# Kernel optimization log

Measured on AMD Instinct MI355X. Metric: run time of the kernel, lower is better.

Reference implementation:

```python
import jax, jax.numpy as jnp
from jax import lax
import numpy as np

# Config mirroring init_kwargs
B, N, PD = 4, 16384, 3
PROJ = 64                 # projection_channel
M1, K1, C1 = 2048, 32, 128  # level-1 SA: fps points, neighbors, out channel
M2, K2, C2 = 512, 32, 256   # level-2 SA
DH, DO = 512, 256           # dense hidden / out (dense_channels)


def fps(pts, M):
    """Farthest point sampling. pts: [N,3] -> indices [M] (starts at point 0)."""
    n = pts.shape[0]
    def step(carry, _):
        dmin, last = carry
        d = jnp.sum((pts - pts[last]) ** 2, axis=-1)   # dist to newest center
        dmin = jnp.minimum(dmin, d)
        nxt = jnp.argmax(dmin).astype(jnp.int32)
        return (dmin, nxt), last
    init = (jnp.full((n,), 1e10, pts.dtype), jnp.int32(0))
    _, idxs = lax.scan(step, init, None, length=M)
    return idxs


def sa_level(pts, feats, M, K, Wa, ba, Wb, bb):
    """PointNet++ set abstraction: FPS + kNN (xyz space) + grouped MLP + max."""
    idx = jax.vmap(lambda p: fps(p, M))(pts)                       # [B,M]
    centers = jnp.take_along_axis(pts, idx[:, :, None], axis=1)    # [B,M,3]
    d = jnp.sum((centers[:, :, None, :] - pts[:, None, :, :]) ** 2, -1)  # [B,M,N]
    _, nidx = lax.top_k(-d, K)                                      # [B,M,K]
    gather = jax.vmap(lambda a, i: a[i])
    rel = gather(pts, nidx) - centers[:, :, None, :]                # [B,M,K,3]
    nf = gather(feats, nidx)                                        # [B,M,K,C]
    g = jnp.concatenate([rel, nf], axis=-1)                         # use_xyz=True
    h = jax.nn.relu(g @ Wa + ba)
    h = jax.nn.relu(h @ Wb + bb)
    return centers, jnp.max(h, axis=2)                              # [B,M,Cout]


def setup_inputs() -> dict:
    key = jax.random.key(0)
    ks = jax.random.split(key, 12)
    w = lambda k, shape, s: jax.random.normal(k, shape, jnp.float32) * s
    z = lambda c: jnp.zeros((c,), jnp.float32)
    return {
        "xyz": jax.random.normal(ks[0], (B, N, PD), jnp.float32),
        "Wp": w(ks[1], (PD, PROJ), 0.3), "bp": z(PROJ),
        "W1a": w(ks[2], (PROJ + 3, C1), 0.1), "b1a": z(C1),
        "W1b": w(ks[3], (C1, C1), 0.08), "b1b": z(C1),
        "W2a": w(ks[4], (C1 + 3, C2), 0.08), "b2a": z(C2),
        "W2b": w(ks[5], (C2, C2), 0.06), "b2b": z(C2),
        "Wd1": w(ks[6], (2 * C2, DH), 0.05), "bd1": z(DH),
        "Wd2": w(ks[7], (DH, DO), 0.05), "bd2": z(DO),
    }


def reference(xyz, Wp, bp, W1a, b1a, W1b, b1b, W2a, b2a, W2b, b2b,
              Wd1, bd1, Wd2, bd2):
    feats = xyz @ Wp + bp            # point_proj: [B,N,PROJ]
    pts = xyz[..., :3]
    pts, feats = sa_level(pts, feats, M1, K1, W1a, b1a, W1b, b1b)
    pts, feats = sa_level(pts, feats, M2, K2, W2a, b2a, W2b, b2b)
    # global max + avg pool (adaptive_max/avg_pool1d to 1), concat -> [B,2*C2]
    g = jnp.concatenate([jnp.max(feats, axis=1), jnp.mean(feats, axis=1)], -1)
    h = jax.nn.relu(g @ Wd1 + bd1)   # DenseBlock w/ activation
    return h @ Wd2 + bd2             # last block: no activation (last_activation=False)
```

## Files before the change

### kernel.cpp

```cpp
#include <hip/hip_runtime.h>

#define B_    4
#define N1_   16384
#define M1_   2048
#define M2_   512
#define KNN_  32
#define PROJ_ 64
#define C1_   128
#define C2_   256
#define PROJ_BLKS_ ((B_ * N1_ * PROJ_) / 512)
#define KNN_BLKS_  ((M1_ / 64) * (B_ * 64))

__device__ __forceinline__ float sqdist_exact(float px, float py, float pz,
                                              float cx, float cy, float cz) {
    float dx = __fsub_rn(px, cx);
    float dy = __fsub_rn(py, cy);
    float dz = __fsub_rn(pz, cz);
    return __fadd_rn(__fadd_rn(__fmul_rn(dx, dx), __fmul_rn(dy, dy)), __fmul_rn(dz, dz));
}

__device__ __forceinline__ float aload(const float* p) {
    return __uint_as_float(__hip_atomic_load((const unsigned*)p,
                           __ATOMIC_RELAXED, __HIP_MEMORY_SCOPE_AGENT));
}
__device__ __forceinline__ unsigned auload(const unsigned* p) {
    return __hip_atomic_load(p, __ATOMIC_RELAXED, __HIP_MEMORY_SCOPE_AGENT);
}

#define F_PROG1(f,b) ((f) + (b) * 16)
#define F_PROG2(f,b) ((f) + 64 + (b) * 16)
#define F_M2DONE(f,b) ((f) + 128 + (b) * 16)

__global__ void __launch_bounds__(1024)
sortx_kernel(const float* __restrict__ xyz, float* __restrict__ sx,
             float* __restrict__ sy, float* __restrict__ sz,
             float* __restrict__ sp) {
    const int b = blockIdx.x, t = threadIdx.x;
    const int lane = t & 63, w = t >> 6;
    const float* P = xyz + (size_t)b * N1_ * 3;
    __shared__ int hist[1024];
    __shared__ int wsum[16];
    hist[t] = 0;
    __syncthreads();
    for (int j = t; j < N1_; j += 1024) {
        unsigned kb = __float_as_uint(P[j * 3]);
        kb ^= (kb >> 31) ? 0xFFFFFFFFu : 0x80000000u;
        atomicAdd(&hist[kb >> 22], 1);
    }
    __syncthreads();
    int v = hist[t];
    int cum = v;
    for (int off = 1; off < 64; off <<= 1) {
        int o = __shfl_up(cum, off);
        if (lane >= off) cum += o;
    }
    if (lane == 63) wsum[w] = cum;
    __syncthreads();
    int wpre = 0;
    for (int i = 0; i < w; ++i) wpre += wsum[i];
    const int excl = cum - v + wpre;
    __syncthreads();
    hist[t] = excl;
    __syncthreads();
    for (int j = t; j < N1_; j += 1024) {
        float x = P[j * 3], y = P[j * 3 + 1], z = P[j * 3 + 2];
        unsigned kb = __float_as_uint(x);
        kb ^= (kb >> 31) ? 0xFFFFFFFFu : 0x80000000u;
        int pos = atomicAdd(&hist[kb >> 22], 1);
        size_t o = (size_t)b * N1_ + pos;
        sx[o] = x; sy[o] = y; sz[o] = z;
        float* pr = sp + ((size_t)b * N1_ + pos) * 3;
        pr[0] = x; pr[1] = y; pr[2] = z;
    }
}

typedef float v2f __attribute__((ext_vector_type(2)));

template<int CTRL, int RM>
__device__ __forceinline__ unsigned long long dpp_umax64(unsigned long long pk) {
    unsigned lo = (unsigned)__builtin_amdgcn_update_dpp(
        0, (int)(unsigned)pk, CTRL, RM, 0xf, true);
    unsigned hi = (unsigned)__builtin_amdgcn_update_dpp(
        0, (int)(unsigned)(pk >> 32), CTRL, RM, 0xf, true);
    unsigned long long o = ((unsigned long long)hi << 32) | (unsigned long long)lo;
    return (o > pk) ? o : pk;
}

__device__ __forceinline__ unsigned long long wave_max_key(unsigned long long pk) {
    pk = dpp_umax64<0x111, 0xf>(pk);
    pk = dpp_umax64<0x112, 0xf>(pk);
    pk = dpp_umax64<0x114, 0xf>(pk);
    pk = dpp_umax64<0x118, 0xf>(pk);
    pk = dpp_umax64<0x142, 0xa>(pk);
    pk = dpp_umax64<0x143, 0xc>(pk);
    return pk;
}

__device__ __forceinline__ unsigned reduce8_widx(const unsigned long long* wk,
                                                 int lane) {
    unsigned long long k8 = wk[lane & 7];
    k8 = dpp_umax64<0x111, 0xf>(k8);
    k8 = dpp_umax64<0x112, 0xf>(k8);
    k8 = dpp_umax64<0x114, 0xf>(k8);
    unsigned lo = (unsigned)__builtin_amdgcn_readlane((int)(unsigned)k8, 7);
    return ~lo;
}

__device__ __forceinline__ unsigned reduce2_widx(const unsigned long long* wk,
                                                 int lane) {
    unsigned long long k2 = wk[lane & 1];
    k2 = dpp_umax64<0x111, 0xf>(k2);
    unsigned lo = (unsigned)__builtin_amdgcn_readlane((int)(unsigned)k2, 1);
    return ~lo;
}

template<int N, int NT>
__device__ void knn_bodyT(const float* __restrict__ P,
                          float cx, float cy, float cz,
                          int* __restrict__ out, char* arena) {
    constexpr int K = KNN_;
    constexpr int CAP = 224;
    const int t = threadIdx.x;
    const int lane = t & 63;
    const int w = t >> 6;

    int*      hist = (int*)arena;
    unsigned* eqk  = (unsigned*)(arena + 8192);
    int*      eqi  = (int*)(arena + 8192 + 896);
    int*      wsum = (int*)(arena + 8192 + 1792);
    int*      ctrl = (int*)(arena + 8192 + 1824);

    unsigned prefix = 0; int pbits = 0;
    unsigned Tlo = 0; unsigned long long Thi = 0x100000000ull;
    int L = 0, target = K, Cbin = N;

    for (int round = 0; round < 3; ++round) {
        const int bits  = (round < 2) ? 11 : 10;
        const int nbins = 1 << bits;
        const int shift = 32 - pbits - bits;
        for (int i = t; i < nbins; i += NT) hist[i] = 0;
        __syncthreads();
        for (int j = t; j < N; j += NT) {
            float d = sqdist_exact(P[j * 3], P[j * 3 + 1], P[j * 3 + 2], cx, cy, cz);
            unsigned key = __float_as_uint(d);
            if (key >= Tlo && (unsigned long long)key < Thi)
                atomicAdd(&hist[(key >> shift) & (nbins - 1)], 1);
        }
        __syncthreads();
        const int per = nbins / NT;
        int s = 0;
        for (int i = 0; i < per; ++i) s += hist[t * per + i];
        int cum = s;
        for (int off = 1; off < 64; off <<= 1) {
            int o = __shfl_up(cum, off);
            if (lane >= off) cum += o;
        }
        if (lane == 63) wsum[w] = cum;
        __syncthreads();
        int wpre = 0;
        for (int i = 0; i < w; ++i) wpre += wsum[i];
        cum += wpre;
        const int cumex = cum - s;
        if ((cumex < target) && (cum >= target)) {
            int acc = cumex;
            for (int i = 0; i < per; ++i) {
                int h = hist[t * per + i];
                if (acc + h >= target) { ctrl[2] = t * per + i; ctrl[3] = acc; ctrl[4] = h; break; }
                acc += h;
            }
        }
        __syncthreads();
        const int binsel = ctrl[2];
        const int Ladd   = ctrl[3];
        const int bincnt = ctrl[4];
        L += Ladd;
        target -= Ladd;
        prefix = (prefix << bits) | (unsigned)binsel;
        pbits += bits;
        Tlo = prefix << (32 - pbits);
        Thi = ((unsigned long long)prefix + 1ull) << (32 - pbits);
        Cbin = bincnt;
        __syncthreads();
        if (Cbin <= CAP) break;
    }

    if (t == 0) { ctrl[0] = 0; ctrl[1] = 0; }
    __syncthreads();

    if (Cbin <= CAP) {
        for (int j = t; j < N; j += NT) {
            float d = sqdist_exact(P[j * 3], P[j * 3 + 1], P[j * 3 + 2], cx, cy, cz);
            unsigned key = __float_as_uint(d);
            if (key < Tlo) {
                int p = atomicAdd(&ctrl[0], 1);
                out[p] = j;
            } else if ((unsigned long long)key < Thi) {
                int p = atomicAdd(&ctrl[1], 1);
                eqk[p] = key; eqi[p] = j;
            }
        }
        __syncthreads();
        const int E = ctrl[1];
        for (int e = t; e < E; e += NT) {
            unsigned ke = eqk[e]; int ie = eqi[e];
            int rank = 0;
            for (int f = 0; f < E; ++f) {
                unsigned kf = eqk[f]; int jf = eqi[f];
                rank += (kf < ke || (kf == ke && jf < ie)) ? 1 : 0;
            }
            if (rank < target) out[L + rank] = ie;
        }
    } else {
        if (t < 64) {
            int cnt = 0;
            for (int jb = 0; jb < N; jb += 64) {
                int j = jb + lane;
                float d = sqdist_exact(P[j * 3], P[j * 3 + 1], P[j * 3 + 2], cx, cy, cz);
                unsigned key = __float_as_uint(d);
                if (key < Tlo) {
                    int p = atomicAdd(&ctrl[0], 1);
                    out[p] = j;
                }
                bool eq = (key == Tlo);
                unsigned long long mb = __ballot(eq);
                int below = __popcll(mb & ((1ull << lane) - 1ull));
                if (eq && (cnt + below) < target) out[L + cnt + below] = j;
                cnt += (int)__popcll(mb);
            }
        }
    }
}

__global__ __attribute__((amdgpu_flat_work_group_size(512, 512)))
__attribute__((amdgpu_waves_per_eu(2, 2)))
void mega1_kernel(const float* __restrict__ xyz,
                  const float* __restrict__ sx, const float* __restrict__ sy,
                  const float* __restrict__ sz, const float* __restrict__ sp,
                  const float* __restrict__ Wp, const float* __restrict__ bp,
                  float* __restrict__ feats0, float* __restrict__ centers1,
                  int* __restrict__ nidx1, unsigned* __restrict__ prog) {
#pragma clang fp contract(off)
    __shared__ alignas(16) char arena[24832];
    asm volatile("" ::: "v255");
    const int bid = blockIdx.x;
    const int t = threadIdx.x;

    if (bid >= B_ + PROJ_BLKS_) {
        const int k = bid - (B_ + PROJ_BLKS_);
        const int c = k >> 8;
        const int b = (k >> 6) & 3;
        const int m = c * 64 + (k & 63);
        if (t == 0) {
            while (auload(F_PROG1(prog, b)) <= (unsigned)c)
                __builtin_amdgcn_s_sleep(16);
        }
        __syncthreads();
        const float* cw = centers1 + ((size_t)b * M1_ + m) * 3;
        float cx = aload(cw + 0), cy = aload(cw + 1), cz = aload(cw + 2);
        knn_bodyT<N1_, 512>(xyz + (size_t)b * N1_ * 3, cx, cy, cz,
                            nidx1 + ((size_t)b * M1_ + m) * KNN_, arena);
        return;
    }
    if (bid >= B_) {
        int tid = (bid - B_) * 512 + t;
        int cc = tid & (PROJ_ - 1);
        int pn = tid >> 6;
        const float* p = xyz + (size_t)pn * 3;
        float acc = p[0] * Wp[0 * PROJ_ + cc];
        acc = __fmaf_rn(p[1], Wp[1 * PROJ_ + cc], acc);
        acc = __fmaf_rn(p[2], Wp[2 * PROJ_ + cc], acc);
        feats0[tid] = acc + bp[cc];
        return;
    }
    constexpr int NT = 512;
    constexpr int NW = NT / 64;
    constexpr int PPT = N1_ / NT;
    const int b = bid;
    const int w = t >> 6;
    const int lane = t & 63;
    const float* P  = xyz + (size_t)b * N1_ * 3;
    const float* SX = sx + (size_t)b * N1_;
    const float* SY = sy + (size_t)b * N1_;
    const float* SZ = sz + (size_t)b * N1_;
    const float* SP = sp + (size_t)b * N1_ * 3;
    float* C1 = centers1 + (size_t)b * M1_ * 3;
    const int base = t * PPT;
    const unsigned nbase = ~(unsigned)base;

    unsigned long long (*wkey)[NW] = (unsigned long long(*)[NW])arena;
    float* cb1 = (float*)(arena + 128);

    float px[PPT], py[PPT], pz[PPT], dmin[PPT];
#pragma unroll
    for (int k = 0; k < PPT; ++k) {
        px[k] = SX[base + k];
        py[k] = SY[base + k];
        pz[k] = SZ[base + k];
        dmin[k] = 1e10f;
    }
#pragma unroll
    for (int k = 0; k < PPT; ++k)
        asm volatile("" : "+v"(px[k]), "+v"(py[k]), "+v"(pz[k]), "+v"(dmin[k]));

    float xlo = px[0], xhi = px[0];
#pragma unroll
    for (int k = 1; k < PPT; ++k) {
        xlo = fminf(xlo, px[k]);
        xhi = fmaxf(xhi, px[k]);
    }
    for (int off = 1; off < 64; off <<= 1) {
        xlo = fminf(xlo, __shfl_xor(xlo, off));
        xhi = fmaxf(xhi, __shfl_xor(xhi, off));
    }

    unsigned long long mykey = ((unsigned long long)__float_as_uint(1e10f) << 32);
    float cx = P[0], cy = P[1], cz = P[2];

    for (int m = 0; m < M1_; ++m) {
        if (t == 0) {
            cb1[m * 3 + 0] = cx; cb1[m * 3 + 1] = cy; cb1[m * 3 + 2] = cz;
        }
        if ((m & 63) == 63) {
            __syncthreads();
            const int c = m >> 6;
            if (t < 48)
                ((float4*)C1)[c * 48 + t] = ((const float4*)cb1)[c * 48 + t];
            __syncthreads();
            if (t == 0)
                __hip_atomic_store(F_PROG1(prog, b), (unsigned)(c + 1),
                                   __ATOMIC_RELEASE, __HIP_MEMORY_SCOPE_AGENT);
        }
        if (m == M1_ - 1) break;
        const int par = m & 1;
        const float UBval = __uint_as_float((unsigned)(mykey >> 32));
        const float dxs = fmaxf(fmaxf(xlo - cx, cx - xhi), 0.0f);
        if (!(0.999f * (dxs * dxs) >= UBval)) {
            unsigned long long pk = 0;
#pragma unroll
            for (int k = 0; k < PPT; ++k) {
                float d  = sqdist_exact(px[k], py[k], pz[k], cx, cy, cz);
                float nd = fminf(dmin[k], d);
                dmin[k] = nd;
                unsigned long long kk =
                    ((unsigned long long)__float_as_uint(nd) << 32) |
                    (unsigned)(nbase - (unsigned)k);
                pk = (kk > pk) ? kk : pk;
            }
            pk = wave_max_key(pk);
            unsigned klo = (unsigned)__builtin_amdgcn_readlane((int)(unsigned)pk, 63);
            unsigned khi = (unsigned)__builtin_amdgcn_readlane((int)(unsigned)(pk >> 32), 63);
            mykey = ((unsigned long long)khi << 32) | klo;
        }
        if (lane == 63) wkey[par][w] = mykey;
        __syncthreads();
        const unsigned widx = reduce8_widx(wkey[par], lane);
        const float* cp = SP + (size_t)widx * 3;
        cx = cp[0]; cy = cp[1]; cz = cp[2];
    }
}

__device__ __forceinline__ void fps2_body(const float* __restrict__ centers1,
                                          float* __restrict__ centers2,
                                          unsigned* __restrict__ prog,
                                          char* arena) {
#pragma clang fp contract(off)
    constexpr int NT = 128;
    constexpr int NW = 2;
    constexpr int NP = (M1_ / NT) / 2;
    const int b = blockIdx.x;
    const int t = threadIdx.x;
    const int w = t >> 6;
    const int lane = t & 63;
    const float* P = centers1 + (size_t)b * M1_ * 3;
    float* C = centers2 + (size_t)b * M2_ * 3;

    unsigned long long (*wkey)[NW] = (unsigned long long(*)[NW])arena;
    float* cb2 = (float*)(arena + 64);

    v2f px2[NP], py2[NP], pz2[NP];
    float dmin[2 * NP];
#pragma unroll
    for (int p = 0; p < NP; ++p) {
        const int j0 = (2 * p) * NT + t;
        const int j1 = j0 + NT;
        px2[p] = (v2f){P[j0 * 3 + 0], P[j1 * 3 + 0]};
        py2[p] = (v2f){P[j0 * 3 + 1], P[j1 * 3 + 1]};
        pz2[p] = (v2f){P[j0 * 3 + 2], P[j1 * 3 + 2]};
        dmin[2 * p] = 1e10f; dmin[2 * p + 1] = 1e10f;
    }
#pragma unroll
    for (int p = 0; p < NP; ++p)
        asm volatile("" : "+v"(px2[p]), "+v"(py2[p]), "+v"(pz2[p]));

    float cx = P[0], cy = P[1], cz = P[2];

    for (int m = 0; m < M2_; ++m) {
        if (t == 0) {
            cb2[m * 3 + 0] = cx; cb2[m * 3 + 1] = cy; cb2[m * 3 + 2] = cz;
        }
        if ((m & 63) == 63) {
            __syncthreads();
            const int c = m >> 6;
            if (t < 48)
                ((float4*)C)[c * 48 + t] = ((const float4*)cb2)[c * 48 + t];
            __syncthreads();
            if (t == 0)
                __hip_atomic_store(F_PROG2(prog, b), (unsigned)(c + 1),
                                   __ATOMIC_RELEASE, __HIP_MEMORY_SCOPE_AGENT);
        }
        if (m == M2_ - 1) break;
        const int par = m & 1;
        const v2f c2x = {cx, cx}, c2y = {cy, cy}, c2z = {cz, cz};
        float bv = -1.0f; int bk = 0;
#pragma unroll
        for (int p = 0; p < NP; ++p) {
            v2f dx = px2[p] - c2x;
            v2f dy = py2[p] - c2y;
            v2f dz = pz2[p] - c2z;
            v2f d2 = (dx * dx + dy * dy) + dz * dz;
            float nd0 = fminf(dmin[2 * p],     d2.x);
            float nd1 = fminf(dmin[2 * p + 1], d2.y);
            dmin[2 * p]     = nd0;
            dmin[2 * p + 1] = nd1;
            bool g0 = nd0 > bv; bv = g0 ? nd0 : bv; bk = g0 ? 2 * p     : bk;
            bool g1 = nd1 > bv; bv = g1 ? nd1 : bv; bk = g1 ? 2 * p + 1 : bk;
        }
        unsigned gi = (unsigned)(bk * NT + t);
        unsigned long long pk =
            ((unsigned long long)__float_as_uint(bv) << 32) | (unsigned)(~gi);
        pk = wave_max_key(pk);
        if (lane == 63) wkey[par][w] = pk;
        __syncthreads();
        const unsigned widx = reduce2_widx(wkey[par], lane);
        const float* cp = P + (size_t)widx * 3;
        cx = cp[0]; cy = cp[1]; cz = cp[2];
    }
}

template<int NPTS, int FD, int CO, int M>
__device__ __forceinline__ void mlp_body(int bm, char* arena,
                 const float* __restrict__ pts, const float* __restrict__ feats,
                 const float* __restrict__ centers, const int* __restrict__ nidx,
                 const float* __restrict__ Wa, const float* __restrict__ ba,
                 const float* __restrict__ Wb, const float* __restrict__ bb,
                 float* __restrict__ outf) {
    constexpr int KN = KNN_;
    constexpr int GS = FD + 4;
    const int b = bm / M;
    const int t = threadIdx.x;
    float (*g)[GS]  = (float(*)[GS])arena;
    float (*h1)[CO] = (float(*)[CO])(arena + sizeof(float) * KN * GS);
    const int* nb = nidx + (size_t)bm * KN;
    const float* cen = centers + (size_t)bm * 3;
    const float cx = cen[0], cy = cen[1], cz = cen[2];
    {
        constexpr int PARTS = CO / KN;
        constexpr int CHUNK = FD / PARTS;
        const int kk = t / PARTS;
        const int q  = t % PARTS;
        const int j  = nb[kk];
        const float* f = feats + ((size_t)b * NPTS + j) * FD + q * CHUNK;
        float* gr = &g[kk][q * CHUNK];
#pragma unroll
        for (int u = 0; u < CHUNK / 4; ++u)
            *(float4*)(gr + 4 * u) = *(const float4*)(f + 4 * u);
        if (q == 0) {
            const float* p = pts + ((size_t)b * NPTS + j) * 3;
            g[kk][FD + 0] = __fsub_rn(p[0], cx);
            g[kk][FD + 1] = __fsub_rn(p[1], cy);
            g[kk][FD + 2] = __fsub_rn(p[2], cz);
            g[kk][FD + 3] = 0.f;
        }
    }
    __syncthreads();
    const int o = t;
    float acc[KN];
#pragma unroll
    for (int k = 0; k < KN; ++k) acc[k] = ba[o];
    for (int s4 = 0; s4 < FD / 4; ++s4) {
        const float w0 = Wa[(4 * s4 + 3) * CO + o];
        const float w1 = Wa[(4 * s4 + 4) * CO + o];
        const float w2 = Wa[(4 * s4 + 5) * CO + o];
        const float w3 = Wa[(4 * s4 + 6) * CO + o];
#pragma unroll
        for (int k = 0; k < KN; ++k) {
            float4 gv = *(const float4*)&g[k][4 * s4];
            acc[k] = __fmaf_rn(gv.x, w0, acc[k]);
            acc[k] = __fmaf_rn(gv.y, w1, acc[k]);
            acc[k] = __fmaf_rn(gv.z, w2, acc[k]);
            acc[k] = __fmaf_rn(gv.w, w3, acc[k]);
        }
    }
    {
        const float w0 = Wa[0 * CO + o];
        const float w1 = Wa[1 * CO + o];
        const float w2 = Wa[2 * CO + o];
#pragma unroll
        for (int k = 0; k < KN; ++k) {
            float4 gv = *(const float4*)&g[k][FD];
            acc[k] = __fmaf_rn(gv.x, w0, acc[k]);
            acc[k] = __fmaf_rn(gv.y, w1, acc[k]);
            acc[k] = __fmaf_rn(gv.z, w2, acc[k]);
        }
    }
#pragma unroll
    for (int k = 0; k < KN; ++k) h1[k][o] = fmaxf(acc[k], 0.f);
    __syncthreads();
#pragma unroll
    for (int k = 0; k < KN; ++k) acc[k] = bb[o];
    for (int s4 = 0; s4 < CO / 4; ++s4) {
        const float w0 = Wb[(4 * s4 + 0) * CO + o];
        const float w1 = Wb[(4 * s4 + 1) * CO + o];
        const float w2 = Wb[(4 * s4 + 2) * CO + o];
        const float w3 = Wb[(4 * s4 + 3) * CO + o];
#pragma unroll
        for (int k = 0; k < KN; ++k) {
            float4 hv = *(const float4*)&h1[k][4 * s4];
            acc[k] = __fmaf_rn(hv.x, w0, acc[k]);
            acc[k] = __fmaf_rn(hv.y, w1, acc[k]);
            acc[k] = __fmaf_rn(hv.z, w2, acc[k]);
            acc[k] = __fmaf_rn(hv.w, w3, acc[k]);
        }
    }
    float mx = 0.f;
#pragma unroll
    for (int k = 0; k < KN; ++k) mx = fmaxf(mx, fmaxf(acc[k], 0.f));
    outf[(size_t)bm * CO + o] = mx;
}

__global__ void __launch_bounds__(C1_)
sa1_kernel(const float* __restrict__ xyz, const float* __restrict__ feats0,
           const float* __restrict__ centers1, const int* __restrict__ nidx1,
           const float* __restrict__ W1a, const float* __restrict__ b1a,
           const float* __restrict__ W1b, const float* __restrict__ b1b,
           float* __restrict__ feats1, float* __restrict__ centers2,
           int* __restrict__ nidx2, unsigned* __restrict__ prog) {
    constexpr size_t MLP_BYTES =
        sizeof(float) * (KNN_ * (PROJ_ + 4) + KNN_ * C1_);
    __shared__ alignas(16) char arena[MLP_BYTES];
    const int bid = blockIdx.x;
    const int t = threadIdx.x;
    if (bid < B_) {
        fps2_body(centers1, centers2, prog, arena);
        return;
    }
    if (bid < B_ + B_ * M1_) {
        mlp_body<N1_, PROJ_, C1_, M1_>(bid - B_, arena, xyz, feats0,
                                       centers1, nidx1, W1a, b1a, W1b, b1b, feats1);
        return;
    }
    const int k = bid - (B_ + B_ * M1_);
    const int c = k >> 8;
    const int b = (k >> 6) & 3;
    const int m = c * 64 + (k & 63);
    if (t == 0) {
        while (auload(F_PROG2(prog, b)) <= (unsigned)c)
            __builtin_amdgcn_s_sleep(16);
    }
    __syncthreads();
    const float* cw = centers2 + ((size_t)b * M2_ + m) * 3;
    float cx = aload(cw + 0), cy = aload(cw + 1), cz = aload(cw + 2);
    knn_bodyT<M1_, 128>(centers1 + (size_t)b * M1_ * 3, cx, cy, cz,
                        nidx2 + ((size_t)b * M2_ + m) * KNN_, arena);
}

__global__ void __launch_bounds__(C2_)
mlp2_head_kernel(const float* __restrict__ centers1, const float* __restrict__ feats1,
                 const float* __restrict__ centers2, const int* __restrict__ nidx2,
                 const float* __restrict__ W2a, const float* __restrict__ b2a,
                 const float* __restrict__ W2b, const float* __restrict__ b2b,
                 const float* __restrict__ Wd1, const float* __restrict__ bd1,
                 const float* __restrict__ Wd2, const float* __restrict__ bd2,
                 float* __restrict__ feats2, float* __restrict__ outp,
                 unsigned* __restrict__ prog) {
    constexpr size_t BYTES = sizeof(float) * (KNN_ * (C1_ + 4) + KNN_ * C2_);
    __shared__ alignas(16) char arena[BYTES];
    const int bid = blockIdx.x;
    const int t = threadIdx.x;
    if (bid < B_ * M2_) {
        mlp_body<M1_, C1_, C2_, M2_>(bid, arena, centers1, feats1,
                                     centers2, nidx2, W2a, b2a, W2b, b2b, feats2);
        __syncthreads();
        if (t == 0) {
            const int b = bid / M2_;
            __hip_atomic_fetch_add(F_M2DONE(prog, b), 1u,
                                   __ATOMIC_RELEASE, __HIP_MEMORY_SCOPE_AGENT);
        }
        return;
    }
    const int b = bid - B_ * M2_;
    if (t == 0) {
        while (auload(F_M2DONE(prog, b)) < (unsigned)M2_)
            __builtin_amdgcn_s_sleep(16);
    }
    __syncthreads();
    float* gsh = (float*)arena;
    float* hsh = (float*)(arena + 2048);
    const float* F = feats2 + (size_t)b * M2_ * C2_;
    float mx = -1e30f, sm = 0.f;
    for (int r = 0; r < M2_; ++r) {
        float v = aload(&F[r * C2_ + t]);
        mx = fmaxf(mx, v);
        sm += v;
    }
    gsh[t] = mx;
    gsh[C2_ + t] = sm * (1.0f / (float)M2_);
    __syncthreads();
#pragma unroll
    for (int oo = 0; oo < 2; ++oo) {
        const int o = t + oo * 256;
        float acc = bd1[o];
        for (int i = 0; i < 512; ++i)
            acc = __fmaf_rn(gsh[i], Wd1[i * 512 + o], acc);
        hsh[o] = fmaxf(acc, 0.f);
    }
    __syncthreads();
    float acc = bd2[t];
    for (int i = 0; i < 512; ++i)
        acc = __fmaf_rn(hsh[i], Wd2[i * 256 + t], acc);
    outp[b * 256 + t] = acc;
}

extern "C" void kernel_launch(void* const* d_in, const int* in_sizes, int n_in,
                              void* d_out, int out_size, void* d_ws, size_t ws_size,
                              hipStream_t stream) {
    const float* xyz = (const float*)d_in[0];
    const float* Wp  = (const float*)d_in[1];
    const float* bp  = (const float*)d_in[2];
    const float* W1a = (const float*)d_in[3];
    const float* b1a = (const float*)d_in[4];
    const float* W1b = (const float*)d_in[5];
    const float* b1b = (const float*)d_in[6];
    const float* W2a = (const float*)d_in[7];
    const float* b2a = (const float*)d_in[8];
    const float* W2b = (const float*)d_in[9];
    const float* b2b = (const float*)d_in[10];
    const float* Wd1 = (const float*)d_in[11];
    const float* bd1 = (const float*)d_in[12];
    const float* Wd2 = (const float*)d_in[13];
    const float* bd2 = (const float*)d_in[14];
    float* out = (float*)d_out;

    char* ws = (char*)d_ws;
    size_t off = 0;
    auto alloc = [&](size_t bytes) { void* p = ws + off; off += (bytes + 255) & ~(size_t)255; return p; };
    float* feats0   = (float*)alloc((size_t)B_ * N1_ * PROJ_ * 4);
    float* centers1 = (float*)alloc((size_t)B_ * M1_ * 3 * 4);
    int*   nidx1    = (int*)  alloc((size_t)B_ * M1_ * KNN_ * 4);
    float* feats1   = (float*)alloc((size_t)B_ * M1_ * C1_ * 4);
    float* centers2 = (float*)alloc((size_t)B_ * M2_ * 3 * 4);
    int*   nidx2    = (int*)  alloc((size_t)B_ * M2_ * KNN_ * 4);
    float* feats2   = (float*)alloc((size_t)B_ * M2_ * C2_ * 4);
    unsigned* prog  = (unsigned*)alloc(1024);
    float* sx       = (float*)alloc((size_t)B_ * N1_ * 4);
    float* sy       = (float*)alloc((size_t)B_ * N1_ * 4);
    float* sz       = (float*)alloc((size_t)B_ * N1_ * 4);
    float* sp       = (float*)alloc((size_t)B_ * N1_ * 3 * 4);
    (void)in_sizes; (void)n_in; (void)out_size; (void)ws_size;

    hipMemsetAsync(prog, 0, 1024, stream);

    sortx_kernel<<<dim3(B_), dim3(1024), 0, stream>>>(xyz, sx, sy, sz, sp);
    mega1_kernel<<<dim3(B_ + PROJ_BLKS_ + KNN_BLKS_), dim3(512), 0, stream>>>(
        xyz, sx, sy, sz, sp, Wp, bp, feats0, centers1, nidx1, prog);
    sa1_kernel<<<dim3(B_ + B_ * M1_ + B_ * M2_), dim3(C1_), 0, stream>>>(
        xyz, feats0, centers1, nidx1, W1a, b1a, W1b, b1b, feats1,
        centers2, nidx2, prog);
    mlp2_head_kernel<<<dim3(B_ * M2_ + B_), dim3(C2_), 0, stream>>>(
        centers1, feats1, centers2, nidx2, W2a, b2a, W2b, b2b,
        Wd1, bd1, Wd2, bd2, feats2, out, prog);
}
```

Baseline: 3.232 ms.

## Fuse level-1 MLP into FPS/kNN megakernel and pipeline level-2 kNN with MLP

Moves the level-1 grouped MLP into the mega1 kernel as 512-thread blocks. Each block waits on a per-chunk kNN completion counter and a projection-done counter, so MLP work overlaps the ongoing FPS and kNN instead of waiting for a kernel boundary. Level-2 FPS, kNN and MLP now share one kernel with chunk-level flags, and level-2 FPS and kNN use 256 threads. This removes a kernel launch and the serialization between stages. In exchange it adds many spin-wait blocks that hold CU slots and depend on forward-progress ordering of block dispatch.

```diff
diff --git a/kernel.cpp b/kernel.cpp
--- a/kernel.cpp
+++ b/kernel.cpp
@@ -9,7 +9,7 @@
 #define C1_   128
 #define C2_   256
 #define PROJ_BLKS_ ((B_ * N1_ * PROJ_) / 512)
-#define KNN_BLKS_  ((M1_ / 64) * (B_ * 64))
+#define TAIL_BLKS_ (32 * 512)
 
 __device__ __forceinline__ float sqdist_exact(float px, float py, float pz,
                                               float cx, float cy, float cz) {
@@ -26,10 +26,16 @@
 __device__ __forceinline__ unsigned auload(const unsigned* p) {
     return __hip_atomic_load(p, __ATOMIC_RELAXED, __HIP_MEMORY_SCOPE_AGENT);
 }
-
-#define F_PROG1(f,b) ((f) + (b) * 16)
-#define F_PROG2(f,b) ((f) + 64 + (b) * 16)
-#define F_M2DONE(f,b) ((f) + 128 + (b) * 16)
+__device__ __forceinline__ void afence() {
+    __builtin_amdgcn_fence(__ATOMIC_ACQUIRE, "agent");
+}
+
+#define F_PROG1(f,b)  ((f) + (b) * 16)
+#define F_PROG2(f,b)  ((f) + 64 + (b) * 16)
+#define F_PROJD(f)    ((f) + 128)
+#define F_K1D(f,b,c)  ((f) + 192 + ((b) * 32 + (c)) * 16)
+#define F_M2D(f,b)    ((f) + 2240 + (b) * 16)
+#define F_K2D(f,b,c)  ((f) + 2304 + ((b) * 8 + (c)) * 16)
 
 __global__ void __launch_bounds__(1024)
 sortx_kernel(const float* __restrict__ xyz, float* __restrict__ sx,
@@ -106,11 +112,12 @@
     return ~lo;
 }
 
-__device__ __forceinline__ unsigned reduce2_widx(const unsigned long long* wk,
+__device__ __forceinline__ unsigned reduce4_widx(const unsigned long long* wk,
                                                  int lane) {
-    unsigned long long k2 = wk[lane & 1];
-    k2 = dpp_umax64<0x111, 0xf>(k2);
-    unsigned lo = (unsigned)__builtin_amdgcn_readlane((int)(unsigned)k2, 1);
+    unsigned long long k4 = wk[lane & 3];
+    k4 = dpp_umax64<0x111, 0xf>(k4);
+    k4 = dpp_umax64<0x112, 0xf>(k4);
+    unsigned lo = (unsigned)__builtin_amdgcn_readlane((int)(unsigned)k4, 3);
     return ~lo;
 }
 
@@ -231,34 +238,149 @@
     }
 }
 
+__device__ void mlp1_512(int b, int m, char* arena,
+                         const float* __restrict__ xyz,
+                         const float* __restrict__ feats0,
+                         const float* __restrict__ centers1,
+                         const int* __restrict__ nidx1,
+                         const float* __restrict__ Wa, const float* __restrict__ ba,
+                         const float* __restrict__ Wb, const float* __restrict__ bb,
+                         float* __restrict__ feats1) {
+    constexpr int KN = KNN_, FD = PROJ_, CO = C1_, GS = FD + 4;
+    const int t = threadIdx.x;
+    const size_t bm = (size_t)b * M1_ + m;
+    float (*g)[GS]  = (float(*)[GS])arena;
+    float (*h1)[CO] = (float(*)[CO])(arena + 8704);
+    float (*pm)[CO] = (float(*)[CO])(arena + 8704 + 16384);
+    const int* nb = nidx1 + bm * KN;
+    const float* cen = centers1 + bm * 3;
+    const float cx = cen[0], cy = cen[1], cz = cen[2];
+    {
+        const int kk = t >> 4;
+        const int q  = t & 15;
+        const int j  = nb[kk];
+        const float* f = feats0 + ((size_t)b * N1_ + j) * FD + q * 4;
+        *(float4*)&g[kk][q * 4] = *(const float4*)f;
+        if (q == 0) {
+            const float* p = xyz + ((size_t)b * N1_ + j) * 3;
+            g[kk][FD + 0] = __fsub_rn(p[0], cx);
+            g[kk][FD + 1] = __fsub_rn(p[1], cy);
+            g[kk][FD + 2] = __fsub_rn(p[2], cz);
+            g[kk][FD + 3] = 0.f;
+        }
+    }
+    __syncthreads();
+    const int o = t & (CO - 1);
+    const int grp = t >> 7;
+    const int k0 = grp * 8;
+    float acc[8];
+#pragma unroll
+    for (int k = 0; k < 8; ++k) acc[k] = ba[o];
+    for (int s4 = 0; s4 < FD / 4; ++s4) {
+        const float w0 = Wa[(4 * s4 + 3) * CO + o];
+        const float w1 = Wa[(4 * s4 + 4) * CO + o];
+        const float w2 = Wa[(4 * s4 + 5) * CO + o];
+        const float w3 = Wa[(4 * s4 + 6) * CO + o];
+#pragma unroll
+        for (int k = 0; k < 8; ++k) {
+            float4 gv = *(const float4*)&g[k0 + k][4 * s4];
+            acc[k] = __fmaf_rn(gv.x, w0, acc[k]);
+            acc[k] = __fmaf_rn(gv.y, w1, acc[k]);
+            acc[k] = __fmaf_rn(gv.z, w2, acc[k]);
+            acc[k] = __fmaf_rn(gv.w, w3, acc[k]);
+        }
+    }
+    {
+        const float w0 = Wa[0 * CO + o];
+        const float w1 = Wa[1 * CO + o];
+        const float w2 = Wa[2 * CO + o];
+#pragma unroll
+        for (int k = 0; k < 8; ++k) {
+            float4 gv = *(const float4*)&g[k0 + k][FD];
+            acc[k] = __fmaf_rn(gv.x, w0, acc[k]);
+            acc[k] = __fmaf_rn(gv.y, w1, acc[k]);
+            acc[k] = __fmaf_rn(gv.z, w2, acc[k]);
+        }
+    }
+#pragma unroll
+    for (int k = 0; k < 8; ++k) h1[k0 + k][o] = fmaxf(acc[k], 0.f);
+    __syncthreads();
+#pragma unroll
+    for (int k = 0; k < 8; ++k) acc[k] = bb[o];
+    for (int s4 = 0; s4 < CO / 4; ++s4) {
+        const float w0 = Wb[(4 * s4 + 0) * CO + o];
+        const float w1 = Wb[(4 * s4 + 1) * CO + o];
+        const float w2 = Wb[(4 * s4 + 2) * CO + o];
+        const float w3 = Wb[(4 * s4 + 3) * CO + o];
+#pragma unroll
+        for (int k = 0; k < 8; ++k) {
+            float4 hv = *(const float4*)&h1[k0 + k][4 * s4];
+            acc[k] = __fmaf_rn(hv.x, w0, acc[k]);
+            acc[k] = __fmaf_rn(hv.y, w1, acc[k]);
+            acc[k] = __fmaf_rn(hv.z, w2, acc[k]);
+            acc[k] = __fmaf_rn(hv.w, w3, acc[k]);
+        }
+    }
+    float mx = 0.f;
+#pragma unroll
+    for (int k = 0; k < 8; ++k) mx = fmaxf(mx, fmaxf(acc[k], 0.f));
+    pm[grp][o] = mx;
+    __syncthreads();
+    if (t < CO) {
+        float m0 = fmaxf(fmaxf(pm[0][o], pm[1][o]), fmaxf(pm[2][o], pm[3][o]));
+        feats1[bm * CO + o] = m0;
+    }
+}
+
 __global__ __attribute__((amdgpu_flat_work_group_size(512, 512)))
 __attribute__((amdgpu_waves_per_eu(2, 2)))
 void mega1_kernel(const float* __restrict__ xyz,
                   const float* __restrict__ sx, const float* __restrict__ sy,
                   const float* __restrict__ sz, const float* __restrict__ sp,
                   const float* __restrict__ Wp, const float* __restrict__ bp,
+                  const float* __restrict__ W1a, const float* __restrict__ b1a,
+                  const float* __restrict__ W1b, const float* __restrict__ b1b,
                   float* __restrict__ feats0, float* __restrict__ centers1,
-                  int* __restrict__ nidx1, unsigned* __restrict__ prog) {
+                  int* __restrict__ nidx1, float* __restrict__ feats1,
+                  unsigned* __restrict__ flags) {
 #pragma clang fp contract(off)
-    __shared__ alignas(16) char arena[24832];
+    __shared__ alignas(16) char arena[27136];
     asm volatile("" ::: "v255");
     const int bid = blockIdx.x;
     const int t = threadIdx.x;
 
     if (bid >= B_ + PROJ_BLKS_) {
         const int k = bid - (B_ + PROJ_BLKS_);
-        const int c = k >> 8;
-        const int b = (k >> 6) & 3;
-        const int m = c * 64 + (k & 63);
+        const int c = k >> 9;
+        const int r = k & 511;
+        const int i = r & 255;
+        const int b = (i >> 6) & 3;
+        const int m = c * 64 + (i & 63);
+        if (r < 256) {
+            if (t == 0) {
+                while (auload(F_PROG1(flags, b)) <= (unsigned)c)
+                    __builtin_amdgcn_s_sleep(16);
+            }
+            __syncthreads();
+            const float* cw = centers1 + ((size_t)b * M1_ + m) * 3;
+            float cx = aload(cw + 0), cy = aload(cw + 1), cz = aload(cw + 2);
+            knn_bodyT<N1_, 512>(xyz + (size_t)b * N1_ * 3, cx, cy, cz,
+                                nidx1 + ((size_t)b * M1_ + m) * KNN_, arena);
+            __syncthreads();
+            if (t == 0)
+                __hip_atomic_fetch_add(F_K1D(flags, b, c), 1u,
+                                       __ATOMIC_RELEASE, __HIP_MEMORY_SCOPE_AGENT);
+            return;
+        }
         if (t == 0) {
-            while (auload(F_PROG1(prog, b)) <= (unsigned)c)
+            while (auload(F_K1D(flags, b, c)) < 64u ||
+                   auload(F_PROJD(flags)) < (unsigned)PROJ_BLKS_)
                 __builtin_amdgcn_s_sleep(16);
         }
         __syncthreads();
-        const float* cw = centers1 + ((size_t)b * M1_ + m) * 3;
-        float cx = aload(cw + 0), cy = aload(cw + 1), cz = aload(cw + 2);
-        knn_bodyT<N1_, 512>(xyz + (size_t)b * N1_ * 3, cx, cy, cz,
-                            nidx1 + ((size_t)b * M1_ + m) * KNN_, arena);
+        afence();
+        mlp1_512(b, m, arena, xyz, feats0, centers1, nidx1,
+                 W1a, b1a, W1b, b1b, feats1);
         return;
     }
     if (bid >= B_) {
@@ -270,6 +392,10 @@
         acc = __fmaf_rn(p[1], Wp[1 * PROJ_ + cc], acc);
         acc = __fmaf_rn(p[2], Wp[2 * PROJ_ + cc], acc);
         feats0[tid] = acc + bp[cc];
+        __syncthreads();
+        if (t == 0)
+            __hip_atomic_fetch_add(F_PROJD(flags), 1u,
+                                   __ATOMIC_RELEASE, __HIP_MEMORY_SCOPE_AGENT);
         return;
     }
     constexpr int NT = 512;
@@ -327,7 +453,7 @@
                 ((float4*)C1)[c * 48 + t] = ((const float4*)cb1)[c * 48 + t];
             __syncthreads();
             if (t == 0)
-                __hip_atomic_store(F_PROG1(prog, b), (unsigned)(c + 1),
+                __hip_atomic_store(F_PROG1(flags, b), (unsigned)(c + 1),
                                    __ATOMIC_RELEASE, __HIP_MEMORY_SCOPE_AGENT);
         }
         if (m == M1_ - 1) break;
@@ -361,11 +487,11 @@
 
 __device__ __forceinline__ void fps2_body(const float* __restrict__ centers1,
                                           float* __restrict__ centers2,
-                                          unsigned* __restrict__ prog,
+                                          unsigned* __restrict__ flags,
                                           char* arena) {
 #pragma clang fp contract(off)
-    constexpr int NT = 128;
-    constexpr int NW = 2;
+    constexpr int NT = 256;
+    constexpr int NW = 4;
     constexpr int NP = (M1_ / NT) / 2;
     const int b = blockIdx.x;
     const int t = threadIdx.x;
@@ -405,7 +531,7 @@
                 ((float4*)C)[c * 48 + t] = ((const float4*)cb2)[c * 48 + t];
             __syncthreads();
             if (t == 0)
-                __hip_atomic_store(F_PROG2(prog, b), (unsigned)(c + 1),
+                __hip_atomic_store(F_PROG2(flags, b), (unsigned)(c + 1),
                                    __ATOMIC_RELEASE, __HIP_MEMORY_SCOPE_AGENT);
         }
         if (m == M2_ - 1) break;
@@ -431,7 +557,7 @@
         pk = wave_max_key(pk);
         if (lane == 63) wkey[par][w] = pk;
         __syncthreads();
-        const unsigned widx = reduce2_widx(wkey[par], lane);
+        const unsigned widx = reduce4_widx(wkey[par], lane);
         const float* cp = P + (size_t)widx * 3;
         cx = cp[0]; cy = cp[1]; cz = cp[2];
     }
@@ -528,78 +654,74 @@
     outf[(size_t)bm * CO + o] = mx;
 }
 
-__global__ void __launch_bounds__(C1_)
-sa1_kernel(const float* __restrict__ xyz, const float* __restrict__ feats0,
-           const float* __restrict__ centers1, const int* __restrict__ nidx1,
-           const float* __restrict__ W1a, const float* __restrict__ b1a,
-           const float* __restrict__ W1b, const float* __restrict__ b1b,
-           float* __restrict__ feats1, float* __restrict__ centers2,
-           int* __restrict__ nidx2, unsigned* __restrict__ prog) {
-    constexpr size_t MLP_BYTES =
-        sizeof(float) * (KNN_ * (PROJ_ + 4) + KNN_ * C1_);
-    __shared__ alignas(16) char arena[MLP_BYTES];
-    const int bid = blockIdx.x;
-    const int t = threadIdx.x;
-    if (bid < B_) {
-        fps2_body(centers1, centers2, prog, arena);
-        return;
-    }
-    if (bid < B_ + B_ * M1_) {
-        mlp_body<N1_, PROJ_, C1_, M1_>(bid - B_, arena, xyz, feats0,
-                                       centers1, nidx1, W1a, b1a, W1b, b1b, feats1);
-        return;
-    }
-    const int k = bid - (B_ + B_ * M1_);
-    const int c = k >> 8;
-    const int b = (k >> 6) & 3;
-    const int m = c * 64 + (k & 63);
-    if (t == 0) {
-        while (auload(F_PROG2(prog, b)) <= (unsigned)c)
-            __builtin_amdgcn_s_sleep(16);
-    }
-    __syncthreads();
-    const float* cw = centers2 + ((size_t)b * M2_ + m) * 3;
-    float cx = aload(cw + 0), cy = aload(cw + 1), cz = aload(cw + 2);
-    knn_bodyT<M1_, 128>(centers1 + (size_t)b * M1_ * 3, cx, cy, cz,
-                        nidx2 + ((size_t)b * M2_ + m) * KNN_, arena);
-}
-
 __global__ void __launch_bounds__(C2_)
-mlp2_head_kernel(const float* __restrict__ centers1, const float* __restrict__ feats1,
-                 const float* __restrict__ centers2, const int* __restrict__ nidx2,
-                 const float* __restrict__ W2a, const float* __restrict__ b2a,
-                 const float* __restrict__ W2b, const float* __restrict__ b2b,
-                 const float* __restrict__ Wd1, const float* __restrict__ bd1,
-                 const float* __restrict__ Wd2, const float* __restrict__ bd2,
-                 float* __restrict__ feats2, float* __restrict__ outp,
-                 unsigned* __restrict__ prog) {
+sa2_kernel(const float* __restrict__ centers1, const float* __restrict__ feats1,
+           float* __restrict__ centers2, int* __restrict__ nidx2,
+           const float* __restrict__ W2a, const float* __restrict__ b2a,
+           const float* __restrict__ W2b, const float* __restrict__ b2b,
+           const float* __restrict__ Wd1, const float* __restrict__ bd1,
+           const float* __restrict__ Wd2, const float* __restrict__ bd2,
+           float* __restrict__ feats2, float* __restrict__ outp,
+           unsigned* __restrict__ flags) {
     constexpr size_t BYTES = sizeof(float) * (KNN_ * (C1_ + 4) + KNN_ * C2_);
     __shared__ alignas(16) char arena[BYTES];
     const int bid = blockIdx.x;
     const int t = threadIdx.x;
-    if (bid < B_ * M2_) {
-        mlp_body<M1_, C1_, C2_, M2_>(bid, arena, centers1, feats1,
-                                     centers2, nidx2, W2a, b2a, W2b, b2b, feats2);
-        __syncthreads();
+    if (bid < B_) {
+        fps2_body(centers1, centers2, flags, arena);
+        return;
+    }
+    const int kk = bid - B_;
+    if (kk < 8 * 512) {
+        const int c = kk >> 9;
+        const int r = kk & 511;
+        const int i = r & 255;
+        const int b = (i >> 6) & 3;
+        const int m = c * 64 + (i & 63);
+        if (r < 256) {
+            if (t == 0) {
+                while (auload(F_PROG2(flags, b)) <= (unsigned)c)
+                    __builtin_amdgcn_s_sleep(16);
+            }
+            __syncthreads();
+            const float* cw = centers2 + ((size_t)b * M2_ + m) * 3;
+            float cx = aload(cw + 0), cy = aload(cw + 1), cz = aload(cw + 2);
+            knn_bodyT<M1_, 256>(centers1 + (size_t)b * M1_ * 3, cx, cy, cz,
+                                nidx2 + ((size_t)b * M2_ + m) * KNN_, arena);
+            __syncthreads();
+            if (t == 0)
+                __hip_atomic_fetch_add(F_K2D(flags, b, c), 1u,
+                                       __ATOMIC_RELEASE, __HIP_MEMORY_SCOPE_AGENT);
+            return;
+        }
         if (t == 0) {
-            const int b = bid / M2_;
-            __hip_atomic_fetch_add(F_M2DONE(prog, b), 1u,
+            while (auload(F_K2D(flags, b, c)) < 64u)
+                __builtin_amdgcn_s_sleep(16);
+        }
+        __syncthreads();
+        afence();
+        mlp_body<M1_, C1_, C2_, M2_>((int)((size_t)b * M2_ + m), arena,
+                                     centers1, feats1, centers2, nidx2,
+                                     W2a, b2a, W2b, b2b, feats2);
+        __syncthreads();
+        if (t == 0)
+            __hip_atomic_fetch_add(F_M2D(flags, b), 1u,
                                    __ATOMIC_RELEASE, __HIP_MEMORY_SCOPE_AGENT);
-        }
         return;
     }
-    const int b = bid - B_ * M2_;
+    const int b = kk - 8 * 512;
     if (t == 0) {
-        while (auload(F_M2DONE(prog, b)) < (unsigned)M2_)
+        while (auload(F_M2D(flags, b)) < (unsigned)M2_)
             __builtin_amdgcn_s_sleep(16);
     }
     __syncthreads();
+    afence();
     float* gsh = (float*)arena;
     float* hsh = (float*)(arena + 2048);
     const float* F = feats2 + (size_t)b * M2_ * C2_;
     float mx = -1e30f, sm = 0.f;
     for (int r = 0; r < M2_; ++r) {
-        float v = aload(&F[r * C2_ + t]);
+        float v = F[r * C2_ + t];
         mx = fmaxf(mx, v);
         sm += v;
     }
@@ -651,22 +773,20 @@
     float* centers2 = (float*)alloc((size_t)B_ * M2_ * 3 * 4);
     int*   nidx2    = (int*)  alloc((size_t)B_ * M2_ * KNN_ * 4);
     float* feats2   = (float*)alloc((size_t)B_ * M2_ * C2_ * 4);
-    unsigned* prog  = (unsigned*)alloc(1024);
+    unsigned* flags = (unsigned*)alloc(16384);
     float* sx       = (float*)alloc((size_t)B_ * N1_ * 4);
     float* sy       = (float*)alloc((size_t)B_ * N1_ * 4);
     float* sz       = (float*)alloc((size_t)B_ * N1_ * 4);
     float* sp       = (float*)alloc((size_t)B_ * N1_ * 3 * 4);
     (void)in_sizes; (void)n_in; (void)out_size; (void)ws_size;
 
-    hipMemsetAsync(prog, 0, 1024, stream);
+    hipMemsetAsync(flags, 0, 16384, stream);
 
     sortx_kernel<<<dim3(B_), dim3(1024), 0, stream>>>(xyz, sx, sy, sz, sp);
-    mega1_kernel<<<dim3(B_ + PROJ_BLKS_ + KNN_BLKS_), dim3(512), 0, stream>>>(
-        xyz, sx, sy, sz, sp, Wp, bp, feats0, centers1, nidx1, prog);
-    sa1_kernel<<<dim3(B_ + B_ * M1_ + B_ * M2_), dim3(C1_), 0, stream>>>(
-        xyz, feats0, centers1, nidx1, W1a, b1a, W1b, b1b, feats1,
-        centers2, nidx2, prog);
-    mlp2_head_kernel<<<dim3(B_ * M2_ + B_), dim3(C2_), 0, stream>>>(
+    mega1_kernel<<<dim3(B_ + PROJ_BLKS_ + TAIL_BLKS_), dim3(512), 0, stream>>>(
+        xyz, sx, sy, sz, sp, Wp, bp, W1a, b1a, W1b, b1b,
+        feats0, centers1, nidx1, feats1, flags);
+    sa2_kernel<<<dim3(B_ + 8 * 512 + B_), dim3(C2_), 0, stream>>>(
         centers1, feats1, centers2, nidx2, W2a, b2a, W2b, b2b,
-        Wd1, bd1, Wd2, bd2, feats2, out, prog);
-}
+        Wd1, bd1, Wd2, bd2, feats2, out, flags);
+}
```

Result: faster. 3.152 ms (median of 2 runs) (-2.5%).
